# Kernel tuning notes

Hardware: AMD Instinct MI355X
Metric: run time of the kernel (lower is better)

The kernel has to match this reference:

```python
import jax, jax.numpy as jnp
import numpy as np
import math

B, S, DIM = 2, 2048, 4096
N_HEADS, N_KV_HEADS = 32, 8
HEAD_DIM = DIM // N_HEADS  # 128
N_REP = N_HEADS // N_KV_HEADS  # 4
ROPE_THETA = 10000.0


def setup_inputs() -> dict:
    key = jax.random.key(0)
    ks = jax.random.split(key, 6)
    x = jax.random.normal(ks[0], (B, S, DIM), dtype=jnp.float32)
    wq = jax.random.normal(ks[1], (DIM, DIM), dtype=jnp.float32) * 0.02
    wk = jax.random.normal(ks[2], (N_KV_HEADS * HEAD_DIM, DIM), dtype=jnp.float32) * 0.02
    wv = jax.random.normal(ks[3], (N_KV_HEADS * HEAD_DIM, DIM), dtype=jnp.float32) * 0.02
    wo = jax.random.normal(ks[4], (DIM, DIM), dtype=jnp.float32) * 0.02
    # rotary freqs_cis (seqlen, head_dim//2), represented as cos/sin
    inv_freq = 1.0 / (ROPE_THETA ** (jnp.arange(0, HEAD_DIM, 2, dtype=jnp.float32) / HEAD_DIM))
    angles = jnp.arange(S, dtype=jnp.float32)[:, None] * inv_freq[None, :]  # [S, HEAD_DIM//2]
    freqs_cos = jnp.cos(angles)
    freqs_sin = jnp.sin(angles)
    # additive causal mask [S, S]: 0 on/below diagonal, -inf above
    mask = jnp.where(jnp.tril(jnp.ones((S, S), dtype=bool)), 0.0, -jnp.inf).astype(jnp.float32)
    return {"x": x, "wq": wq, "wk": wk, "wv": wv, "wo": wo,
            "freqs_cos": freqs_cos, "freqs_sin": freqs_sin, "mask": mask}


def _apply_rotary(t, freqs_cos, freqs_sin):
    # t: [B, S, H, HEAD_DIM]; interpret pairs (even, odd) as complex
    t2 = t.reshape(*t.shape[:-1], HEAD_DIM // 2, 2)
    tr, ti = t2[..., 0], t2[..., 1]
    c = freqs_cos[None, :, None, :]  # [1, S, 1, HD/2]
    s = freqs_sin[None, :, None, :]
    out_r = tr * c - ti * s
    out_i = tr * s + ti * c
    return jnp.stack([out_r, out_i], axis=-1).reshape(t.shape)


def reference(x, wq, wk, wv, wo, freqs_cos, freqs_sin, mask):
    bsz, seqlen, _ = x.shape
    xq = (x @ wq.T).reshape(bsz, seqlen, N_HEADS, HEAD_DIM)
    xk = (x @ wk.T).reshape(bsz, seqlen, N_KV_HEADS, HEAD_DIM)
    xv = (x @ wv.T).reshape(bsz, seqlen, N_KV_HEADS, HEAD_DIM)
    xq = _apply_rotary(xq, freqs_cos, freqs_sin)
    xk = _apply_rotary(xk, freqs_cos, freqs_sin)
    # repeat_kv (GQA): [B,S,KV,HD] -> [B,S,KV*N_REP,HD] via repeat_interleave on head axis
    keys = jnp.repeat(xk, N_REP, axis=2)
    values = jnp.repeat(xv, N_REP, axis=2)
    # scores: [B, H, S, S]
    scores = jnp.einsum('bqhd,bkhd->bhqk', xq, keys) / math.sqrt(HEAD_DIM)
    scores = scores + mask[None, None, :, :]
    probs = jax.nn.softmax(scores.astype(jnp.float32), axis=-1).astype(xq.dtype)
    out = jnp.einsum('bhqk,bkhd->bqhd', probs, values).reshape(bsz, seqlen, DIM)
    return out @ wo.T
```

## Files before the change

### kernel.cpp

```cpp
#include <hip/hip_runtime.h>

typedef __bf16 bf16;
typedef __bf16 bf16x4 __attribute__((ext_vector_type(4)));
typedef __bf16 bf16x8 __attribute__((ext_vector_type(8)));
typedef float f32x4 __attribute__((ext_vector_type(4)));

#define BB 2
#define SS 2048
#define DIM 4096
#define KVDIM 1024
#define QKVN (DIM + 2 * KVDIM)
#define NH 32
#define NKV 8
#define HD 128
#define NEGINF (-1e30f)

__device__ __forceinline__ void async16(void* lds, const void* gmem) {
    __builtin_amdgcn_global_load_lds(
        (const __attribute__((address_space(1))) void*)gmem,
        (__attribute__((address_space(3))) void*)lds, 16, 0, 0);
}

__device__ __forceinline__ f32x4 mfma16(bf16x8 a, bf16x8 b, f32x4 c) {
    return __builtin_amdgcn_mfma_f32_16x16x32_bf16(a, b, c, 0, 0, 0);
}

struct DetectArgs { const void* p[7]; int n[7]; };

__global__ void detect_dtypes(DetectArgs a, int* flags) {
    __shared__ int bad;
    const int ti = blockIdx.x;
    if (threadIdx.x == 0) bad = 0;
    __syncthreads();
    const bf16* s = (const bf16*)a.p[ti];
    int n = a.n[ti];
    int take = n < 8192 ? n : 8192;
    int lbad = 0;
    for (int i = threadIdx.x; i < take; i += 256) {
        float f = (float)s[i];
        if (!(f > -1e4f && f < 1e4f)) lbad = 1;
    }
    if (lbad) atomicOr(&bad, 1);
    __syncthreads();
    if (threadIdx.x == 0) flags[ti] = bad;
}

__device__ __forceinline__ void conv8(const void* src, bf16* dst, int rel, int flag) {
    if (flag) {
        const float* s = (const float*)src + (size_t)rel * 8;
        bf16x8 v;
#pragma unroll
        for (int j = 0; j < 8; ++j) v[j] = (bf16)s[j];
        *(bf16x8*)(dst + (size_t)rel * 8) = v;
    } else {
        *(bf16x8*)(dst + (size_t)rel * 8) = *((const bf16x8*)src + rel);
    }
}

__global__ void convert_to_bf16(const void* __restrict__ src, bf16* __restrict__ dst,
                                int n8, const int* __restrict__ flagp) {
    int i = blockIdx.x * 256 + threadIdx.x;
    if (i >= n8) return;
    conv8(src, dst, i, *flagp);
}

struct Conv6 { const void* s[6]; bf16* d[6]; int n[6]; const int* f[6]; };

__global__ void convert6(Conv6 c) {
    int u = blockIdx.x * 256 + threadIdx.x;
#pragma unroll
    for (int i = 0; i < 6; ++i) {
        if (u < c.n[i]) { conv8(c.s[i], c.d[i], u, *c.f[i]); return; }
        u -= c.n[i];
    }
}

#define SBAR()  asm volatile("s_barrier" ::: "memory")
#define LGKM0() asm volatile("s_waitcnt lgkmcnt(0)" ::: "memory")
#define VM4()   asm volatile("s_waitcnt vmcnt(4)" ::: "memory")
#define VM0()   asm volatile("s_waitcnt vmcnt(0)" ::: "memory")

__device__ __forceinline__ void gemm256_core(const bf16* __restrict__ A,
                                             const bf16* __restrict__ B,
                                             int K, int m0, int n0,
                                             f32x4 (&acc)[8][4]) {
    __shared__ bf16 sm[2][4][8192];
    const int t = threadIdx.x;
    const int lane = t & 63;
    const int w = t >> 6;
    const int l15 = lane & 15, quad = lane >> 4;
    const int wm = w >> 2;
    const int wn = w & 3;
    const int axr = l15 & 7;
    const int c0 = (quad ^ axr) * 8;
    const int c1 = ((4 + quad) ^ axr) * 8;
    const int srl = t >> 3;
    const int sch = ((t & 7) ^ (srl & 7)) * 8;
    const size_t Ks = (size_t)K;

    bf16x8 aReg[4][2], bReg[4][2];

#define RD_A(c_, mh) { \
    const bf16* ab = &sm[c_][wm][0] + ((mh) * 64 + l15) * 64; \
    _Pragma("unroll") for (int i = 0; i < 4; ++i) { \
        aReg[i][0] = *(const bf16x8*)(ab + i * 1024 + c0); \
        aReg[i][1] = *(const bf16x8*)(ab + i * 1024 + c1); } }

#define RD_B(c_, nh) { \
    const bf16* bb = &sm[c_][2 + (wn >> 1)][0] + ((wn & 1) * 64 + (nh) * 32 + l15) * 64; \
    _Pragma("unroll") for (int jj = 0; jj < 2; ++jj) { \
        bReg[(nh) * 2 + jj][0] = *(const bf16x8*)(bb + jj * 1024 + c0); \
        bReg[(nh) * 2 + jj][1] = *(const bf16x8*)(bb + jj * 1024 + c1); } }

#define STG(c_, reg_, Mat, rowbase, kt) { \
    bf16* d_ = &sm[c_][reg_][0] + (size_t)t * 8; \
    const bf16* s_ = (Mat) + ((size_t)((rowbase) + srl)) * Ks + (size_t)(kt) * 64 + sch; \
    async16(d_, s_); \
    async16(d_ + 4096, s_ + 64 * Ks); }

#define MM(mh, nh) { \
    _Pragma("unroll") for (int i = 0; i < 4; ++i) \
    _Pragma("unroll") for (int jj = 0; jj < 2; ++jj) { \
        acc[(mh) * 4 + i][(nh) * 2 + jj] = \
            mfma16(aReg[i][0], bReg[(nh) * 2 + jj][0], acc[(mh) * 4 + i][(nh) * 2 + jj]); \
        acc[(mh) * 4 + i][(nh) * 2 + jj] = \
            mfma16(aReg[i][1], bReg[(nh) * 2 + jj][1], acc[(mh) * 4 + i][(nh) * 2 + jj]); } }

    STG(0, 0, A, m0, 0);
    STG(0, 2, B, n0, 0);
    STG(0, 1, A, m0 + 128, 0);
    STG(0, 3, B, n0 + 128, 0);
    STG(1, 2, B, n0, 1);
    STG(1, 0, A, m0, 1);
    VM4(); SBAR();

    const int NT = K >> 6;
    for (int T = 0; T < NT; ++T) {
        const int c = T & 1, nc = c ^ 1;
        const int kt1 = (T + 1 < NT) ? T + 1 : 0;
        const int kt2 = (T + 2 < NT) ? T + 2 : 0;
        RD_A(c, 0); RD_B(c, 0);
        STG(nc, 1, A, m0 + 128, kt1);
        SBAR();
        __builtin_amdgcn_s_setprio(1); MM(0, 0); __builtin_amdgcn_s_setprio(0);
        LGKM0(); SBAR();
        RD_B(c, 1);
        STG(nc, 3, B, n0 + 128, kt1);
        SBAR();
        __builtin_amdgcn_s_setprio(1); MM(0, 1); __builtin_amdgcn_s_setprio(0);
        LGKM0(); SBAR();
        RD_A(c, 1);
        STG(c, 2, B, n0, kt2);
        SBAR();
        __builtin_amdgcn_s_setprio(1); MM(1, 0); __builtin_amdgcn_s_setprio(0);
        LGKM0(); SBAR();
        STG(c, 0, A, m0, kt2);
        SBAR();
        __builtin_amdgcn_s_setprio(1); MM(1, 1); __builtin_amdgcn_s_setprio(0);
        LGKM0(); VM4(); SBAR();
    }
#undef RD_A
#undef RD_B
#undef STG
#undef MM
}

__global__ __launch_bounds__(512, 2)
void gemm_qkv(const bf16* __restrict__ A, const bf16* __restrict__ Bqkv,
              bf16* __restrict__ Qo, bf16* __restrict__ Kc, bf16* __restrict__ Vc,
              int M, int K) {
    const int t = threadIdx.x, lane = t & 63, w = t >> 6;
    const int l15 = lane & 15, quad = lane >> 4;
    const int wm = w >> 2, wn = w & 3;
    const int m0 = blockIdx.y * 256, n0 = blockIdx.x * 256;
    f32x4 acc[8][4] = {};
    gemm256_core(A, Bqkv, K, m0, n0, acc);
    bf16* C;
    int cb;
    size_t ldc;
    if (n0 < DIM)               { C = Qo; cb = n0;                ldc = DIM; }
    else if (n0 < DIM + KVDIM)  { C = Kc; cb = n0 - DIM;          ldc = KVDIM; }
    else                        { C = Vc; cb = n0 - DIM - KVDIM;  ldc = KVDIM; }
#pragma unroll
    for (int i = 0; i < 8; ++i)
#pragma unroll
        for (int j = 0; j < 4; ++j) {
            int col = cb + wn * 64 + j * 16 + l15;
#pragma unroll
            for (int r = 0; r < 4; ++r)
                C[(size_t)(m0 + wm * 128 + i * 16 + quad * 4 + r) * ldc + col] = (bf16)acc[i][j][r];
        }
}

__global__ __launch_bounds__(512, 2)
void gemm_nt_out(const bf16* __restrict__ A, const bf16* __restrict__ B,
                 void* __restrict__ C, int M, int N, int K,
                 const int* __restrict__ flagp) {
    const int t = threadIdx.x, lane = t & 63, w = t >> 6;
    const int l15 = lane & 15, quad = lane >> 4;
    const int wm = w >> 2, wn = w & 3;
    const int m0 = blockIdx.y * 256, n0 = blockIdx.x * 256;
    const int f32out = *flagp;
    f32x4 acc[8][4] = {};
    gemm256_core(A, B, K, m0, n0, acc);
#pragma unroll
    for (int i = 0; i < 8; ++i)
#pragma unroll
        for (int j = 0; j < 4; ++j) {
            int col = n0 + wn * 64 + j * 16 + l15;
#pragma unroll
            for (int r = 0; r < 4; ++r) {
                int row = m0 + wm * 128 + i * 16 + quad * 4 + r;
                if (f32out) ((float*)C)[(size_t)row * N + col] = acc[i][j][r];
                else        ((bf16*)C)[(size_t)row * N + col] = (bf16)acc[i][j][r];
            }
        }
}

__device__ __forceinline__ void rope8(bf16* p, const bf16* fc, const bf16* fs,
                                      int s, int i0, float sc) {
    bf16x8 v = *(bf16x8*)p;
    bf16x8 o;
#pragma unroll
    for (int j = 0; j < 4; ++j) {
        float tr = (float)v[2 * j], ti = (float)v[2 * j + 1];
        float cc = (float)fc[s * 64 + i0 + j];
        float sn = (float)fs[s * 64 + i0 + j];
        o[2 * j]     = (bf16)((tr * cc - ti * sn) * sc);
        o[2 * j + 1] = (bf16)((tr * sn + ti * cc) * sc);
    }
    *(bf16x8*)p = o;
}

#define ROPE_BLOCKS ((DIM * (BB * SS) / 8 + KVDIM * (BB * SS) / 8) / 256)

__global__ void rope_tv(bf16* __restrict__ Q, bf16* __restrict__ Kr,
                        const bf16* __restrict__ fc, const bf16* __restrict__ fs,
                        const bf16* __restrict__ V, bf16* __restrict__ Vt) {
    __shared__ bf16 tile[64][74];
    const int bid = blockIdx.x;
    const int t = threadIdx.x;
    if (bid < ROPE_BLOCKS) {
        const float qscale = 0.08838834764831845f * 1.4426950408889634f;
        int u = bid * 256 + t;
        const int QU = (DIM * (BB * SS)) / 8;
        if (u < QU) {
            int row = u >> 9;
            int c = (u & 511) * 8;
            rope8(Q + (size_t)row * DIM + c, fc, fs, row & (SS - 1), (c >> 1) & 63, qscale);
        } else {
            u -= QU;
            int row = u >> 7;
            int c = (u & 127) * 8;
            rope8(Kr + (size_t)row * KVDIM + c, fc, fs, row & (SS - 1), (c >> 1) & 63, 1.0f);
        }
        return;
    }
    const int b2 = bid - ROPE_BLOCKS;
    const int st = b2 & 31, ct = (b2 >> 5) & 15, b = b2 >> 9;
    const int s0 = st * 64;
    const int kvh = ct >> 1, d0 = (ct & 1) * 64;
#pragma unroll
    for (int i = 0; i < 2; ++i) {
        int o = i * 256 + t;
        int r = o >> 3, c8 = (o & 7) * 8;
        bf16x8 v = *(const bf16x8*)(V + (size_t)(b * SS + s0 + r) * KVDIM + kvh * HD + d0 + c8);
#pragma unroll
        for (int j = 0; j < 8; ++j) tile[r][c8 + j] = v[j];
    }
    __syncthreads();
#pragma unroll
    for (int i = 0; i < 2; ++i) {
        int o = i * 256 + t;
        int sseg = (o & 7) * 8, dl = o >> 3;
        bf16x8 v;
#pragma unroll
        for (int j = 0; j < 8; ++j) v[j] = tile[sseg + j][dl];
        *(bf16x8*)(Vt + ((size_t)((b * NKV + kvh) * HD) + d0 + dl) * SS + s0 + sseg) = v;
    }
}

__global__ __launch_bounds__(256, 2)
void flash_attn(const bf16* __restrict__ Q, const bf16* __restrict__ Kr,
                const bf16* __restrict__ Vt, bf16* __restrict__ AO) {
    __shared__ char smem[32768];
    bf16* Ks  = (bf16*)smem;
    bf16* Vts = (bf16*)(smem + 16384);
    char* Ps  = smem;
    const int t = threadIdx.x, w = t >> 6, lane = t & 63;
    const int l15 = lane & 15, quad = lane >> 4;
    const int bh = blockIdx.x;
    const int b = bh >> 5, h = bh & 31, kvh = h >> 2;
    const int q0 = ((int)gridDim.y - 1 - (int)blockIdx.y) * 128;

    bf16x8 qf[2][4];
#pragma unroll
    for (int mi = 0; mi < 2; ++mi) {
        int qrow = b * SS + q0 + w * 32 + mi * 16 + l15;
#pragma unroll
        for (int ks = 0; ks < 4; ++ks)
            qf[mi][ks] = *(const bf16x8*)(Q + (size_t)qrow * DIM + h * HD + ks * 32 + quad * 8);
    }

    f32x4 of[2][8] = {};
    float mrow[2] = {NEGINF, NEGINF};
    float lrow[2] = {0.f, 0.f};

    const int kend = q0 + 128;
    for (int kk = 0; kk < kend; kk += 64) {
#pragma unroll
        for (int i = 0; i < 4; ++i) {
            int s = i * 256 + t;
            int key = s >> 4, slot = s & 15;
            int dseg = slot ^ (key & 15);
            async16((char*)Ks + (size_t)s * 16,
                    Kr + (size_t)(b * SS + kk + key) * KVDIM + kvh * HD + dseg * 8);
        }
#pragma unroll
        for (int i = 0; i < 4; ++i) {
            int s = i * 256 + t;
            int d = s >> 3, slot = s & 7;
            int kseg = slot ^ (d & 7);
            async16((char*)Vts + (size_t)s * 16,
                    Vt + ((size_t)((b * NKV + kvh) * HD + d)) * SS + kk + kseg * 8);
        }
        VM4(); SBAR();

        f32x4 sacc[2][4] = {};
#pragma unroll
        for (int nt = 0; nt < 4; ++nt) {
            int key = nt * 16 + l15;
#pragma unroll
            for (int ks = 0; ks < 4; ++ks) {
                int slot = (ks * 4 + quad) ^ (key & 15);
                bf16x8 kf = *(const bf16x8*)(Ks + key * 128 + slot * 8);
#pragma unroll
                for (int mi = 0; mi < 2; ++mi)
                    sacc[mi][nt] = mfma16(kf, qf[mi][ks], sacc[mi][nt]);
            }
        }
        if (kk >= q0) {
#pragma unroll
            for (int mi = 0; mi < 2; ++mi) {
                int q = q0 + w * 32 + mi * 16 + l15;
#pragma unroll
                for (int nt = 0; nt < 4; ++nt) {
                    int kbase = kk + nt * 16 + quad * 4;
#pragma unroll
                    for (int r = 0; r < 4; ++r)
                        if (kbase + r > q) sacc[mi][nt][r] = NEGINF;
                }
            }
        }
#pragma unroll
        for (int mi = 0; mi < 2; ++mi) {
            float m01[4];
#pragma unroll
            for (int nt = 0; nt < 4; ++nt)
                m01[nt] = fmaxf(fmaxf(sacc[mi][nt][0], sacc[mi][nt][1]),
                                fmaxf(sacc[mi][nt][2], sacc[mi][nt][3]));
            float mx = fmaxf(fmaxf(m01[0], m01[1]), fmaxf(m01[2], m01[3]));
            mx = fmaxf(mx, __shfl_xor(mx, 16));
            mx = fmaxf(mx, __shfl_xor(mx, 32));
            if (__all(mx - mrow[mi] <= 8.0f)) {
                float rs[4];
#pragma unroll
                for (int nt = 0; nt < 4; ++nt) {
                    rs[nt] = 0.f;
#pragma unroll
                    for (int r = 0; r < 4; ++r) {
                        float p = exp2f(sacc[mi][nt][r] - mrow[mi]);
                        sacc[mi][nt][r] = p;
                        rs[nt] += p;
                    }
                }
                float rsum = (rs[0] + rs[1]) + (rs[2] + rs[3]);
                rsum += __shfl_xor(rsum, 16);
                rsum += __shfl_xor(rsum, 32);
                lrow[mi] += rsum;
            } else {
                float mnew = fmaxf(mrow[mi], mx);
                float alpha = exp2f(mrow[mi] - mnew);
                float rs[4];
#pragma unroll
                for (int nt = 0; nt < 4; ++nt) {
                    rs[nt] = 0.f;
#pragma unroll
                    for (int r = 0; r < 4; ++r) {
                        float p = exp2f(sacc[mi][nt][r] - mnew);
                        sacc[mi][nt][r] = p;
                        rs[nt] += p;
                    }
                }
                float rsum = (rs[0] + rs[1]) + (rs[2] + rs[3]);
                rsum += __shfl_xor(rsum, 16);
                rsum += __shfl_xor(rsum, 32);
                lrow[mi] = lrow[mi] * alpha + rsum;
                mrow[mi] = mnew;
#pragma unroll
                for (int dt = 0; dt < 8; ++dt)
#pragma unroll
                    for (int r = 0; r < 4; ++r) of[mi][dt][r] *= alpha;
            }
        }
        VM0(); SBAR();
#pragma unroll
        for (int mi = 0; mi < 2; ++mi) {
            int row = w * 32 + mi * 16 + l15;
#pragma unroll
            for (int nt = 0; nt < 4; ++nt) {
                bf16x4 pv;
#pragma unroll
                for (int r = 0; r < 4; ++r) pv[r] = (bf16)sacc[mi][nt][r];
                int cc = nt * 2 + (quad >> 1);
                *(bf16x4*)(Ps + row * 128 + ((cc ^ (row & 7)) * 16 + (quad & 1) * 8)) = pv;
            }
        }
#pragma unroll
        for (int kb = 0; kb < 2; ++kb) {
            bf16x8 pa[2];
#pragma unroll
            for (int mi = 0; mi < 2; ++mi) {
                int row = w * 32 + mi * 16 + l15;
                pa[mi] = *(const bf16x8*)(Ps + row * 128 + (((kb * 4 + quad) ^ (row & 7)) * 16));
            }
#pragma unroll
            for (int dt = 0; dt < 8; ++dt) {
                int d = dt * 16 + l15;
                int slot = (kb * 4 + quad) ^ (d & 7);
                bf16x8 vb = *(const bf16x8*)(Vts + d * 64 + slot * 8);
#pragma unroll
                for (int mi = 0; mi < 2; ++mi)
                    of[mi][dt] = mfma16(vb, pa[mi], of[mi][dt]);
            }
        }
        SBAR();
    }
    bf16* Os = (bf16*)smem;
#pragma unroll
    for (int mi = 0; mi < 2; ++mi) {
        float inv = 1.0f / lrow[mi];
        int row = w * 32 + mi * 16 + l15;
#pragma unroll
        for (int dt = 0; dt < 8; ++dt) {
            bf16x4 o4;
#pragma unroll
            for (int r = 0; r < 4; ++r) o4[r] = (bf16)(of[mi][dt][r] * inv);
            int s = dt * 2 + (quad >> 1);
            int slot = s ^ l15;
            *(bf16x4*)((char*)Os + row * 256 + slot * 16 + (quad & 1) * 8) = o4;
        }
    }
    __syncthreads();
#pragma unroll
    for (int i = 0; i < 8; ++i) {
        int flat = i * 256 + t;
        int ql = flat >> 4, s = flat & 15;
        bf16x8 v = *(const bf16x8*)((char*)Os + ql * 256 + (s ^ (ql & 15)) * 16);
        *(bf16x8*)(AO + (size_t)(b * SS + q0 + ql) * DIM + h * HD + s * 8) = v;
    }
}

extern "C" void kernel_launch(void* const* d_in, const int* in_sizes, int n_in,
                              void* d_out, int out_size, void* d_ws, size_t ws_size,
                              hipStream_t stream) {
    const size_t MD = (size_t)BB * SS * DIM;
    const size_t KV = (size_t)BB * SS * KVDIM;
    const size_t WQKV = (size_t)QKVN * DIM;
    const size_t FC = (size_t)SS * (HD / 2);
    const int M = BB * SS;

    int* flags = (int*)d_ws;
    bf16* xb  = (bf16*)((char*)d_ws + 32);
    bf16* wb  = xb + MD;
    bf16* Q   = wb + WQKV;
    bf16* Kr  = Q + MD;
    bf16* Vw  = Kr + KV;
    bf16* Vt  = Vw + KV;
    bf16* fcb = Vt + KV;
    bf16* fsb = fcb + FC;

    DetectArgs da;
    for (int i = 0; i < 7; ++i) { da.p[i] = d_in[i]; da.n[i] = in_sizes[i]; }
    detect_dtypes<<<7, 256, 0, stream>>>(da, flags);

    dim3 blk(256);
    dim3 blk512(512);

    {
        Conv6 c;
        c.s[0] = d_in[0]; c.d[0] = xb;            c.n[0] = (int)(MD / 8); c.f[0] = flags + 0;
        c.s[1] = d_in[1]; c.d[1] = wb;            c.n[1] = (int)(MD / 8); c.f[1] = flags + 1;
        c.s[2] = d_in[2]; c.d[2] = wb + MD;       c.n[2] = (int)(KV / 8); c.f[2] = flags + 2;
        c.s[3] = d_in[3]; c.d[3] = wb + MD + KV;  c.n[3] = (int)(KV / 8); c.f[3] = flags + 3;
        c.s[4] = d_in[5]; c.d[4] = fcb;           c.n[4] = (int)(FC / 8); c.f[4] = flags + 5;
        c.s[5] = d_in[6]; c.d[5] = fsb;           c.n[5] = (int)(FC / 8); c.f[5] = flags + 6;
        long total = 2L * (MD / 8) + 2L * (KV / 8) + 2L * (FC / 8);
        convert6<<<(int)((total + 255) / 256), blk, 0, stream>>>(c);
    }

    gemm_qkv<<<dim3(QKVN / 256, M / 256), blk512, 0, stream>>>(xb, wb, Q, Kr, Vw, M, DIM);

    rope_tv<<<dim3(ROPE_BLOCKS + (SS / 64) * 16 * BB), blk, 0, stream>>>(Q, Kr, fcb, fsb, Vw, Vt);

    flash_attn<<<dim3(BB * NH, SS / 128), blk, 0, stream>>>(Q, Kr, Vt, xb);

    convert_to_bf16<<<(int)(MD / 8 / 256), blk, 0, stream>>>(d_in[4], wb, (int)(MD / 8), flags + 4);
    gemm_nt_out<<<dim3(DIM / 256, M / 256), blk512, 0, stream>>>(xb, wb, d_out, M, DIM, DIM, flags + 0);
}
```

Measured before the change: 711.4 us.

## Fuse RoPE and V transpose into split Q and KV GEMM epilogues

Splits the combined QKV projection into separate Q and KV GEMMs and applies rotary embedding (with the softmax scale for Q) directly in the GEMM epilogues using lane shuffles to pair even/odd columns. V is written transposed straight from the KV GEMM epilogue. This removes the standalone rope/transpose kernel and its extra global read/write of Q, K and V. In exchange there is an additional kernel launch, and the KV GEMM grid is smaller, which may underfill the device.

```diff
diff --git a/kernel.cpp b/kernel.cpp
--- a/kernel.cpp
+++ b/kernel.cpp
@@ -9,7 +9,6 @@
 #define SS 2048
 #define DIM 4096
 #define KVDIM 1024
-#define QKVN (DIM + 2 * KVDIM)
 #define NH 32
 #define NKV 8
 #define HD 128
@@ -166,30 +165,84 @@
 }
 
 __global__ __launch_bounds__(512, 2)
-void gemm_qkv(const bf16* __restrict__ A, const bf16* __restrict__ Bqkv,
-              bf16* __restrict__ Qo, bf16* __restrict__ Kc, bf16* __restrict__ Vc,
-              int M, int K) {
+void gemm_q(const bf16* __restrict__ A, const bf16* __restrict__ B,
+            bf16* __restrict__ Qo, const bf16* __restrict__ fc,
+            const bf16* __restrict__ fs, int M, int K) {
     const int t = threadIdx.x, lane = t & 63, w = t >> 6;
     const int l15 = lane & 15, quad = lane >> 4;
     const int wm = w >> 2, wn = w & 3;
     const int m0 = blockIdx.y * 256, n0 = blockIdx.x * 256;
     f32x4 acc[8][4] = {};
-    gemm256_core(A, Bqkv, K, m0, n0, acc);
-    bf16* C;
-    int cb;
-    size_t ldc;
-    if (n0 < DIM)               { C = Qo; cb = n0;                ldc = DIM; }
-    else if (n0 < DIM + KVDIM)  { C = Kc; cb = n0 - DIM;          ldc = KVDIM; }
-    else                        { C = Vc; cb = n0 - DIM - KVDIM;  ldc = KVDIM; }
+    gemm256_core(A, B, K, m0, n0, acc);
+    const float qscale = 0.08838834764831845f * 1.4426950408889634f;
 #pragma unroll
     for (int i = 0; i < 8; ++i)
 #pragma unroll
         for (int j = 0; j < 4; ++j) {
-            int col = cb + wn * 64 + j * 16 + l15;
-#pragma unroll
-            for (int r = 0; r < 4; ++r)
-                C[(size_t)(m0 + wm * 128 + i * 16 + quad * 4 + r) * ldc + col] = (bf16)acc[i][j][r];
-        }
+            int col = n0 + wn * 64 + j * 16 + l15;
+            int fi = (col >> 1) & 63;
+            int par = col & 1;
+#pragma unroll
+            for (int r = 0; r < 4; ++r) {
+                int row = m0 + wm * 128 + i * 16 + quad * 4 + r;
+                int srow = row & (SS - 1);
+                float v = acc[i][j][r];
+                float pv = __shfl_xor(v, 1);
+                float cc = (float)fc[srow * 64 + fi];
+                float sn = (float)fs[srow * 64 + fi];
+                float o = par ? (v * cc + pv * sn) : (v * cc - pv * sn);
+                Qo[(size_t)row * DIM + col] = (bf16)(o * qscale);
+            }
+        }
+}
+
+__global__ __launch_bounds__(512, 2)
+void gemm_kv(const bf16* __restrict__ A, const bf16* __restrict__ Bkv,
+             bf16* __restrict__ Kc, bf16* __restrict__ Vt,
+             const bf16* __restrict__ fc, const bf16* __restrict__ fs,
+             int M, int K) {
+    const int t = threadIdx.x, lane = t & 63, w = t >> 6;
+    const int l15 = lane & 15, quad = lane >> 4;
+    const int wm = w >> 2, wn = w & 3;
+    const int m0 = blockIdx.y * 256, n0 = blockIdx.x * 256;
+    f32x4 acc[8][4] = {};
+    gemm256_core(A, Bkv, K, m0, n0, acc);
+    if (n0 < KVDIM) {
+#pragma unroll
+        for (int i = 0; i < 8; ++i)
+#pragma unroll
+            for (int j = 0; j < 4; ++j) {
+                int col = n0 + wn * 64 + j * 16 + l15;
+                int fi = (col >> 1) & 63;
+                int par = col & 1;
+#pragma unroll
+                for (int r = 0; r < 4; ++r) {
+                    int row = m0 + wm * 128 + i * 16 + quad * 4 + r;
+                    int srow = row & (SS - 1);
+                    float v = acc[i][j][r];
+                    float pv = __shfl_xor(v, 1);
+                    float cc = (float)fc[srow * 64 + fi];
+                    float sn = (float)fs[srow * 64 + fi];
+                    float o = par ? (v * cc + pv * sn) : (v * cc - pv * sn);
+                    Kc[(size_t)row * KVDIM + col] = (bf16)o;
+                }
+            }
+    } else {
+#pragma unroll
+        for (int i = 0; i < 8; ++i)
+#pragma unroll
+            for (int j = 0; j < 4; ++j) {
+                int col = (n0 - KVDIM) + wn * 64 + j * 16 + l15;
+                int kvh = col >> 7, d = col & 127;
+                int row0 = m0 + wm * 128 + i * 16 + quad * 4;
+                int b = row0 >> 11;
+                int s = row0 & (SS - 1);
+                bf16x4 v4;
+#pragma unroll
+                for (int r = 0; r < 4; ++r) v4[r] = (bf16)acc[i][j][r];
+                *(bf16x4*)(Vt + ((size_t)((b * NKV + kvh) * HD + d)) * SS + s) = v4;
+            }
+    }
 }
 
 __global__ __launch_bounds__(512, 2)
@@ -215,69 +268,6 @@
                 else        ((bf16*)C)[(size_t)row * N + col] = (bf16)acc[i][j][r];
             }
         }
-}
-
-__device__ __forceinline__ void rope8(bf16* p, const bf16* fc, const bf16* fs,
-                                      int s, int i0, float sc) {
-    bf16x8 v = *(bf16x8*)p;
-    bf16x8 o;
-#pragma unroll
-    for (int j = 0; j < 4; ++j) {
-        float tr = (float)v[2 * j], ti = (float)v[2 * j + 1];
-        float cc = (float)fc[s * 64 + i0 + j];
-        float sn = (float)fs[s * 64 + i0 + j];
-        o[2 * j]     = (bf16)((tr * cc - ti * sn) * sc);
-        o[2 * j + 1] = (bf16)((tr * sn + ti * cc) * sc);
-    }
-    *(bf16x8*)p = o;
-}
-
-#define ROPE_BLOCKS ((DIM * (BB * SS) / 8 + KVDIM * (BB * SS) / 8) / 256)
-
-__global__ void rope_tv(bf16* __restrict__ Q, bf16* __restrict__ Kr,
-                        const bf16* __restrict__ fc, const bf16* __restrict__ fs,
-                        const bf16* __restrict__ V, bf16* __restrict__ Vt) {
-    __shared__ bf16 tile[64][74];
-    const int bid = blockIdx.x;
-    const int t = threadIdx.x;
-    if (bid < ROPE_BLOCKS) {
-        const float qscale = 0.08838834764831845f * 1.4426950408889634f;
-        int u = bid * 256 + t;
-        const int QU = (DIM * (BB * SS)) / 8;
-        if (u < QU) {
-            int row = u >> 9;
-            int c = (u & 511) * 8;
-            rope8(Q + (size_t)row * DIM + c, fc, fs, row & (SS - 1), (c >> 1) & 63, qscale);
-        } else {
-            u -= QU;
-            int row = u >> 7;
-            int c = (u & 127) * 8;
-            rope8(Kr + (size_t)row * KVDIM + c, fc, fs, row & (SS - 1), (c >> 1) & 63, 1.0f);
-        }
-        return;
-    }
-    const int b2 = bid - ROPE_BLOCKS;
-    const int st = b2 & 31, ct = (b2 >> 5) & 15, b = b2 >> 9;
-    const int s0 = st * 64;
-    const int kvh = ct >> 1, d0 = (ct & 1) * 64;
-#pragma unroll
-    for (int i = 0; i < 2; ++i) {
-        int o = i * 256 + t;
-        int r = o >> 3, c8 = (o & 7) * 8;
-        bf16x8 v = *(const bf16x8*)(V + (size_t)(b * SS + s0 + r) * KVDIM + kvh * HD + d0 + c8);
-#pragma unroll
-        for (int j = 0; j < 8; ++j) tile[r][c8 + j] = v[j];
-    }
-    __syncthreads();
-#pragma unroll
-    for (int i = 0; i < 2; ++i) {
-        int o = i * 256 + t;
-        int sseg = (o & 7) * 8, dl = o >> 3;
-        bf16x8 v;
-#pragma unroll
-        for (int j = 0; j < 8; ++j) v[j] = tile[sseg + j][dl];
-        *(bf16x8*)(Vt + ((size_t)((b * NKV + kvh) * HD) + d0 + dl) * SS + s0 + sseg) = v;
-    }
 }
 
 __global__ __launch_bounds__(256, 2)
@@ -466,17 +456,16 @@
                               hipStream_t stream) {
     const size_t MD = (size_t)BB * SS * DIM;
     const size_t KV = (size_t)BB * SS * KVDIM;
-    const size_t WQKV = (size_t)QKVN * DIM;
     const size_t FC = (size_t)SS * (HD / 2);
     const int M = BB * SS;
 
     int* flags = (int*)d_ws;
     bf16* xb  = (bf16*)((char*)d_ws + 32);
-    bf16* wb  = xb + MD;
-    bf16* Q   = wb + WQKV;
+    bf16* wq  = xb + MD;
+    bf16* wkv = wq + MD;
+    bf16* Q   = wkv + 2 * KV;
     bf16* Kr  = Q + MD;
-    bf16* Vw  = Kr + KV;
-    bf16* Vt  = Vw + KV;
+    bf16* Vt  = Kr + KV;
     bf16* fcb = Vt + KV;
     bf16* fsb = fcb + FC;
 
@@ -489,22 +478,22 @@
 
     {
         Conv6 c;
-        c.s[0] = d_in[0]; c.d[0] = xb;            c.n[0] = (int)(MD / 8); c.f[0] = flags + 0;
-        c.s[1] = d_in[1]; c.d[1] = wb;            c.n[1] = (int)(MD / 8); c.f[1] = flags + 1;
-        c.s[2] = d_in[2]; c.d[2] = wb + MD;       c.n[2] = (int)(KV / 8); c.f[2] = flags + 2;
-        c.s[3] = d_in[3]; c.d[3] = wb + MD + KV;  c.n[3] = (int)(KV / 8); c.f[3] = flags + 3;
-        c.s[4] = d_in[5]; c.d[4] = fcb;           c.n[4] = (int)(FC / 8); c.f[4] = flags + 5;
-        c.s[5] = d_in[6]; c.d[5] = fsb;           c.n[5] = (int)(FC / 8); c.f[5] = flags + 6;
+        c.s[0] = d_in[0]; c.d[0] = xb;       c.n[0] = (int)(MD / 8); c.f[0] = flags + 0;
+        c.s[1] = d_in[1]; c.d[1] = wq;       c.n[1] = (int)(MD / 8); c.f[1] = flags + 1;
+        c.s[2] = d_in[2]; c.d[2] = wkv;      c.n[2] = (int)(KV / 8); c.f[2] = flags + 2;
+        c.s[3] = d_in[3]; c.d[3] = wkv + KV; c.n[3] = (int)(KV / 8); c.f[3] = flags + 3;
+        c.s[4] = d_in[5]; c.d[4] = fcb;      c.n[4] = (int)(FC / 8); c.f[4] = flags + 5;
+        c.s[5] = d_in[6]; c.d[5] = fsb;      c.n[5] = (int)(FC / 8); c.f[5] = flags + 6;
         long total = 2L * (MD / 8) + 2L * (KV / 8) + 2L * (FC / 8);
         convert6<<<(int)((total + 255) / 256), blk, 0, stream>>>(c);
     }
 
-    gemm_qkv<<<dim3(QKVN / 256, M / 256), blk512, 0, stream>>>(xb, wb, Q, Kr, Vw, M, DIM);
-
-    rope_tv<<<dim3(ROPE_BLOCKS + (SS / 64) * 16 * BB), blk, 0, stream>>>(Q, Kr, fcb, fsb, Vw, Vt);
+    gemm_q<<<dim3(DIM / 256, M / 256), blk512, 0, stream>>>(xb, wq, Q, fcb, fsb, M, DIM);
+
+    gemm_kv<<<dim3(2 * KVDIM / 256, M / 256), blk512, 0, stream>>>(xb, wkv, Kr, Vt, fcb, fsb, M, DIM);
 
     flash_attn<<<dim3(BB * NH, SS / 128), blk, 0, stream>>>(Q, Kr, Vt, xb);
 
-    convert_to_bf16<<<(int)(MD / 8 / 256), blk, 0, stream>>>(d_in[4], wb, (int)(MD / 8), flags + 4);
-    gemm_nt_out<<<dim3(DIM / 256, M / 256), blk512, 0, stream>>>(xb, wb, d_out, M, DIM, DIM, flags + 0);
-}
+    convert_to_bf16<<<(int)(MD / 8 / 256), blk, 0, stream>>>(d_in[4], wq, (int)(MD / 8), flags + 4);
+    gemm_nt_out<<<dim3(DIM / 256, M / 256), blk512, 0, stream>>>(xb, wq, d_out, M, DIM, DIM, flags + 0);
+}
```

Result: slower. 728.9 us (+2.5%).
